# Performance work log

Measured on AMD Instinct MI355X. Metric: run time of the kernel, lower is better.

## Reference

```python
import jax, jax.numpy as jnp
import numpy as np
import math

BIG, SMALL, HEADS, FF_MULT = 4096, 256, 4, 2
HEAD_DIM = SMALL // HEADS
FF = SMALL * FF_MULT
EPS = 1.1920929e-07  # torch.nn.RMSNorm default eps=None -> finfo(float32).eps


def rmsnorm(x, g):
    var = jnp.mean(x * x, axis=-1, keepdims=True)
    return x * jax.lax.rsqrt(var + EPS) * g


def setup_inputs() -> dict:
    key = jax.random.key(0)
    ks = jax.random.split(key, 10)
    B, T = 4, 2048
    def lin(k, out_d, in_d):
        # torch nn.Linear default init: U(-1/sqrt(in), 1/sqrt(in)), weight shape (out, in)
        lim = 1.0 / math.sqrt(in_d)
        return jax.random.uniform(k, (out_d, in_d), jnp.float32, -lim, lim)
    return {
        "x": jax.random.normal(ks[0], (B, T, BIG), jnp.float32),
        "W_down": lin(ks[1], SMALL, BIG),
        "W_up": lin(ks[2], BIG, SMALL),
        "W_qkv": lin(ks[3], 3 * SMALL, SMALL),
        "W_o": lin(ks[4], SMALL, SMALL),
        "W_gate": lin(ks[5], FF, SMALL),
        "W_upff": lin(ks[6], FF, SMALL),
        "W_downff": lin(ks[7], SMALL, FF),
        "g1": jnp.ones((SMALL,), jnp.float32),
        "g2": jnp.ones((SMALL,), jnp.float32),
    }


def reference(x, W_down, W_up, W_qkv, W_o, W_gate, W_upff, W_downff, g1, g2):
    B, T, _ = x.shape
    h = x @ W_down.T                                     # (B,T,small)
    hn = rmsnorm(h, g1)
    qkv = (hn @ W_qkv.T).reshape(B, T, 3, HEADS, HEAD_DIM)
    qkv = jnp.transpose(qkv, (2, 0, 3, 1, 4))            # (3,B,H,T,hd)
    q, k, v = qkv[0], qkv[1], qkv[2]
    scores = jnp.einsum('bhqd,bhkd->bhqk', q, k) / math.sqrt(HEAD_DIM)
    causal = jnp.tril(jnp.ones((T, T), bool))
    scores = jnp.where(causal, scores, -jnp.inf)
    attn = jax.nn.softmax(scores, axis=-1)
    out = jnp.einsum('bhqk,bhkd->bhqd', attn, v)
    out = jnp.transpose(out, (0, 2, 1, 3)).reshape(B, T, SMALL)
    h = h + out @ W_o.T
    hn = rmsnorm(h, g2)
    ff = (jax.nn.silu(hn @ W_gate.T) * (hn @ W_upff.T)) @ W_downff.T
    h = h + ff
    return h @ W_up.T                                    # (B,T,big)
```

## Files before the change

### kernel.cpp

```cpp
#include <hip/hip_runtime.h>
#include <hip/hip_bf16.h>

typedef __bf16 bf16x8 __attribute__((ext_vector_type(8)));
typedef __bf16 bf16x4 __attribute__((ext_vector_type(4)));
typedef float f32x4 __attribute__((ext_vector_type(4)));

#define MFMA_BF16(a, b, c) __builtin_amdgcn_mfma_f32_16x16x32_bf16((a), (b), (c), 0, 0, 0)

__device__ __forceinline__ void g2lds16(void* lds, const void* g) {
  __builtin_amdgcn_global_load_lds(
      (const __attribute__((address_space(1))) void*)g,
      (__attribute__((address_space(3))) void*)lds, 16, 0, 0);
}

enum { EP_BF16 = 0, EP_F32 = 1, EP_ADD_F32 = 2, EP_ADD_BF16OUT = 3 };

template <int EPI, int MT, bool SPLITK = false>
__global__ __launch_bounds__(256, 2) void gemm_nt_kernel(
    const __bf16* __restrict__ A, const __bf16* __restrict__ B, const int K,
    __bf16* __restrict__ Co, float* __restrict__ Cf, const int ldc)
{
  __shared__ __align__(16) __bf16 As[2][MT * 32];
  __shared__ __align__(16) __bf16 Bs[2][128 * 32];
  const int tid = threadIdx.x;
  const int wv = tid >> 6, lane = tid & 63;
  const int r16 = lane & 15, g4 = lane >> 4;
  const int row0 = blockIdx.y * MT, col0 = blockIdx.x * 128;
  const int wr = (MT == 128) ? (wv >> 1) * 64 : 0;
  const int wc = (MT == 128) ? (wv & 1) * 64 : wv * 32;
  constexpr int NW = (MT == 128) ? 4 : 2;
  constexpr int NA = (MT == 128) ? 2 : 1;
  const int kz0 = SPLITK ? blockIdx.z * 1024 : 0;

  f32x4 acc[4][NW];
#pragma unroll
  for (int m = 0; m < 4; ++m)
#pragma unroll
    for (int n = 0; n < NW; ++n) acc[m][n] = f32x4{0.f, 0.f, 0.f, 0.f};

  auto stage = [&](int buf, int k0) {
#pragma unroll
    for (int rr = 0; rr < NA; ++rr) {
      const int u = rr * 256 + tid, row = u >> 2, cg = ((u & 3) ^ (row & 3)) * 8;
      g2lds16(&As[buf][u * 8], A + (size_t)(row0 + row) * K + k0 + cg);
    }
#pragma unroll
    for (int rr = 0; rr < 2; ++rr) {
      const int u = rr * 256 + tid, row = u >> 2, cg = ((u & 3) ^ (row & 3)) * 8;
      g2lds16(&Bs[buf][u * 8], B + (size_t)(col0 + row) * K + k0 + cg);
    }
  };

  const int nk = SPLITK ? 32 : (K >> 5);
  const int csw = (g4 ^ (r16 & 3)) * 8;
  int cur = 0;
  stage(0, kz0);
  __syncthreads();

  for (int t = 0; t < nk; ++t) {
    if (t + 1 < nk) stage(cur ^ 1, kz0 + (t + 1) * 32);
    bf16x8 af[4], bfr[NW];
#pragma unroll
    for (int m = 0; m < 4; ++m)
      af[m] = *(const bf16x8*)&As[cur][(wr + m * 16 + r16) * 32 + csw];
#pragma unroll
    for (int n = 0; n < NW; ++n)
      bfr[n] = *(const bf16x8*)&Bs[cur][(wc + n * 16 + r16) * 32 + csw];
#pragma unroll
    for (int m = 0; m < 4; ++m)
#pragma unroll
      for (int n = 0; n < NW; ++n)
        acc[m][n] = MFMA_BF16(af[m], bfr[n], acc[m][n]);
    __syncthreads();
    cur ^= 1;
  }

  const size_t zoff = SPLITK ? (size_t)blockIdx.z * 2097152 : 0;
#pragma unroll
  for (int m = 0; m < 4; ++m)
#pragma unroll
    for (int n = 0; n < NW; ++n)
#pragma unroll
      for (int r = 0; r < 4; ++r) {
        const int row = row0 + wr + m * 16 + g4 * 4 + r;
        const int col = col0 + wc + n * 16 + r16;
        const size_t idx = (size_t)row * ldc + col;
        const float v = acc[m][n][r];
        if constexpr (EPI == EP_BF16) Co[zoff + idx] = (__bf16)v;
        else if constexpr (EPI == EP_F32) __builtin_nontemporal_store(v, &Cf[idx]);
        else if constexpr (EPI == EP_ADD_F32) Cf[idx] += v;
        else Co[idx] = (__bf16)(Cf[idx] + v);
      }
}

__global__ __launch_bounds__(256, 2) void gemm_wo_kernel(
    const __bf16* __restrict__ opart, const float* __restrict__ lpart,
    const __bf16* __restrict__ B, float* __restrict__ Cf)
{
  __shared__ __align__(16) __bf16 As[2][64 * 32];
  __shared__ __align__(16) __bf16 Bs[2][128 * 32];
  const int tid = threadIdx.x;
  const int wv = tid >> 6, lane = tid & 63;
  const int r16 = lane & 15, g4 = lane >> 4;
  const int row0 = blockIdx.y * 64, col0 = blockIdx.x * 128;
  const int wc = wv * 32;

  f32x4 acc[4][2];
#pragma unroll
  for (int m = 0; m < 4; ++m)
#pragma unroll
    for (int n = 0; n < 2; ++n) acc[m][n] = f32x4{0.f, 0.f, 0.f, 0.f};

  const int arow = tid >> 2;
  const int R = row0 + arow;
  const int b = R >> 11, rr_ = R & 2047;
  const int qb = rr_ >> 6, rloc = rr_ & 63;
  const int cgrp = ((tid & 3) ^ (arow & 3)) * 8;

  auto stageA = [&](int buf, int t) {
    const int hh = t >> 1;
    const int dbase = (t & 1) * 32 + cgrp;
    const size_t pb = ((size_t)((b * 4 + hh) * 32 + qb)) * 2;
    const bf16x8 o0 = *(const bf16x8*)(opart + pb * 4096 + rloc * 64 + dbase);
    const bf16x8 o1 = *(const bf16x8*)(opart + (pb + 1) * 4096 + rloc * 64 + dbase);
    const float inv = 1.f / (lpart[pb * 64 + rloc] + lpart[(pb + 1) * 64 + rloc]);
    bf16x8 w;
#pragma unroll
    for (int j = 0; j < 8; ++j) w[j] = (__bf16)(((float)o0[j] + (float)o1[j]) * inv);
    *(bf16x8*)&As[buf][tid * 8] = w;
  };
  auto stageB = [&](int buf, int k0) {
#pragma unroll
    for (int rr = 0; rr < 2; ++rr) {
      const int u = rr * 256 + tid, row = u >> 2, cg = ((u & 3) ^ (row & 3)) * 8;
      g2lds16(&Bs[buf][u * 8], B + (size_t)(col0 + row) * 256 + k0 + cg);
    }
  };

  const int csw = (g4 ^ (r16 & 3)) * 8;
  int cur = 0;
  stageA(0, 0);
  stageB(0, 0);
  __syncthreads();

  for (int t = 0; t < 8; ++t) {
    if (t + 1 < 8) { stageA(cur ^ 1, t + 1); stageB(cur ^ 1, (t + 1) * 32); }
    bf16x8 af[4], bfr[2];
#pragma unroll
    for (int m = 0; m < 4; ++m)
      af[m] = *(const bf16x8*)&As[cur][(m * 16 + r16) * 32 + csw];
#pragma unroll
    for (int n = 0; n < 2; ++n)
      bfr[n] = *(const bf16x8*)&Bs[cur][(wc + n * 16 + r16) * 32 + csw];
#pragma unroll
    for (int m = 0; m < 4; ++m)
#pragma unroll
      for (int n = 0; n < 2; ++n)
        acc[m][n] = MFMA_BF16(af[m], bfr[n], acc[m][n]);
    __syncthreads();
    cur ^= 1;
  }

#pragma unroll
  for (int m = 0; m < 4; ++m)
#pragma unroll
    for (int n = 0; n < 2; ++n)
#pragma unroll
      for (int r = 0; r < 4; ++r) {
        const int row = row0 + m * 16 + g4 * 4 + r;
        const int col = col0 + wc + n * 16 + r16;
        Cf[(size_t)row * 256 + col] += acc[m][n][r];
      }
}

__global__ void cvt_x_kernel(const float* __restrict__ src, __bf16* __restrict__ dst)
{
  const int stride = gridDim.x * 256;
  for (size_t i = (size_t)blockIdx.x * 256 + threadIdx.x; i < 8388608; i += stride) {
    const f32x4 v = *(const f32x4*)(src + i * 4);
    bf16x4 o;
#pragma unroll
    for (int j = 0; j < 4; ++j) o[j] = (__bf16)v[j];
    *(bf16x4*)(dst + i * 4) = o;
  }
}

__global__ void rmsnorm_reduce_kernel(const __bf16* __restrict__ part, const float* __restrict__ g,
                                      float* __restrict__ h, __bf16* __restrict__ out)
{
  const int wv = threadIdx.x >> 6, lane = threadIdx.x & 63;
  const size_t row = (size_t)blockIdx.x * 4 + wv;
  const size_t i = row * 256 + lane * 4;
  f32x4 v = {0.f, 0.f, 0.f, 0.f};
#pragma unroll
  for (int z = 0; z < 4; ++z) {
    const bf16x4 p = *(const bf16x4*)(part + (size_t)z * 2097152 + i);
#pragma unroll
    for (int j = 0; j < 4; ++j) v[j] += (float)p[j];
  }
  *(f32x4*)(h + i) = v;
  float s = v[0] * v[0] + v[1] * v[1] + v[2] * v[2] + v[3] * v[3];
#pragma unroll
  for (int off = 1; off < 64; off <<= 1) s += __shfl_xor(s, off);
  const float scale = rsqrtf(s * (1.f / 256.f) + 1.1920929e-07f);
  const f32x4 gv = *(const f32x4*)(g + lane * 4);
  bf16x4 o;
#pragma unroll
  for (int j = 0; j < 4; ++j) o[j] = (__bf16)(v[j] * scale * gv[j]);
  *(bf16x4*)(out + i) = o;
}

__global__ void rmsnorm_kernel(const float* __restrict__ h, const float* __restrict__ g,
                               __bf16* __restrict__ out)
{
  const int wv = threadIdx.x >> 6, lane = threadIdx.x & 63;
  const size_t row = (size_t)blockIdx.x * 4 + wv;
  const f32x4 v = *(const f32x4*)(h + row * 256 + lane * 4);
  float s = v[0] * v[0] + v[1] * v[1] + v[2] * v[2] + v[3] * v[3];
#pragma unroll
  for (int off = 1; off < 64; off <<= 1) s += __shfl_xor(s, off);
  const float scale = rsqrtf(s * (1.f / 256.f) + 1.1920929e-07f);
  const f32x4 gv = *(const f32x4*)(g + lane * 4);
  bf16x4 o;
#pragma unroll
  for (int j = 0; j < 4; ++j) o[j] = (__bf16)(v[j] * scale * gv[j]);
  *(bf16x4*)(out + row * 256 + lane * 4) = o;
}

struct CvtPack { const float* s[7]; __bf16* d[7]; int n[7]; };
__global__ void cvt_all_kernel(CvtPack p)
{
  int i = (blockIdx.x * 256 + threadIdx.x) * 4;
#pragma unroll
  for (int k = 0; k < 7; ++k) {
    if (i < p.n[k]) {
      const f32x4 v = *(const f32x4*)(p.s[k] + i);
      bf16x4 o;
#pragma unroll
      for (int j = 0; j < 4; ++j) o[j] = (__bf16)v[j];
      *(bf16x4*)(p.d[k] + i) = o;
      return;
    }
    i -= p.n[k];
  }
}

__global__ void silumul_kernel(const __bf16* __restrict__ gu, __bf16* __restrict__ out)
{
  const int gid = blockIdx.x * 256 + threadIdx.x;
  const int row = gid >> 6, k = (gid & 63) * 8;
  const bf16x8 gv = *(const bf16x8*)(gu + (size_t)row * 1024 + k);
  const bf16x8 uv = *(const bf16x8*)(gu + (size_t)row * 1024 + 512 + k);
  bf16x8 ov;
#pragma unroll
  for (int j = 0; j < 8; ++j) {
    const float x = (float)gv[j];
    ov[j] = (__bf16)((x / (1.f + __expf(-x))) * (float)uv[j]);
  }
  *(bf16x8*)(out + (size_t)row * 512 + k) = ov;
}

__global__ __launch_bounds__(256, 4) void attn_kernel(
    const __bf16* __restrict__ qkv, __bf16* __restrict__ opart, float* __restrict__ lpart)
{
  const int bh = blockIdx.x;
  const int by = blockIdx.y;
  const int qb = (by < 16) ? (31 - by) : (by - 16);
  const int z = blockIdx.z;
  const int b = bh >> 2, hh = bh & 3;
  const int tid = threadIdx.x, wv = tid >> 6, lane = tid & 63;
  const int r16 = lane & 15, g4 = lane >> 4;
  const __bf16* base = qkv + (size_t)b * 2048 * 768;
  const int q0 = qb * 64;

  __shared__ __align__(16) __bf16 Ks[2][64 * 64];
  __shared__ __align__(16) __bf16 Vt[64 * 72];
  __shared__ __align__(16) __bf16 Ps[4][16 * 72];

  bf16x8 qf[2];
  {
    const __bf16* qrow = base + (size_t)(q0 + wv * 16 + r16) * 768 + hh * 64;
    qf[0] = *(const bf16x8*)(qrow + g4 * 8);
    qf[1] = *(const bf16x8*)(qrow + 32 + g4 * 8);
  }

  f32x4 oacc[4];
#pragma unroll
  for (int t = 0; t < 4; ++t) oacc[t] = f32x4{0.f, 0.f, 0.f, 0.f};
  float lsum[4] = {0.f, 0.f, 0.f, 0.f};

  auto stageK = [&](int buf, int kv0) {
#pragma unroll
    for (int rr = 0; rr < 2; ++rr) {
      const int u = rr * 256 + tid;
      const int kv = u >> 3, c = u & 7;
      g2lds16(&Ks[buf][u * 8],
              base + (size_t)(kv0 + kv) * 768 + 256 + hh * 64 + ((c ^ (kv & 7)) * 8));
    }
  };
  const int vrow = tid >> 2, vdg = (tid & 3) * 16;
  const int va_ = vrow >> 3, vb_ = vrow & 7;

  bf16x8 v0r, v1r;
  auto loadV = [&](int kv0) {
    const __bf16* vsrc = base + (size_t)(kv0 + vrow) * 768 + 512 + hh * 64 + vdg;
    v0r = *(const bf16x8*)vsrc;
    v1r = *(const bf16x8*)(vsrc + 8);
  };
  auto writeVt = [&]() {
#pragma unroll
    for (int i = 0; i < 8; ++i) {
      int d = vdg + i;
      Vt[d * 72 + ((va_ ^ (d >> 3)) << 3) + vb_] = v0r[i];
      d = vdg + 8 + i;
      Vt[d * 72 + ((va_ ^ (d >> 3)) << 3) + vb_] = v1r[i];
    }
  };

  int c = z, cur = 0;
  const bool any = (c <= qb);
  if (any) { stageK(0, c * 64); loadV(c * 64); }
  __syncthreads();
  if (any) writeVt();
  __syncthreads();

  while (c <= qb) {
    const int nxt = c + 2;
    if (nxt <= qb) { stageK(cur ^ 1, nxt * 64); loadV(nxt * 64); }

    f32x4 sacc[4];
#pragma unroll
    for (int t = 0; t < 4; ++t) sacc[t] = f32x4{0.f, 0.f, 0.f, 0.f};
#pragma unroll
    for (int t = 0; t < 4; ++t)
#pragma unroll
      for (int kk = 0; kk < 2; ++kk) {
        const bf16x8 kf = *(const bf16x8*)
            &Ks[cur][(t * 16 + r16) * 64 + (((kk * 4 + g4) ^ (r16 & 7)) * 8)];
        sacc[t] = MFMA_BF16(qf[kk], kf, sacc[t]);
      }

    const bool diag = (c == qb);
#pragma unroll
    for (int t = 0; t < 4; ++t)
#pragma unroll
      for (int r = 0; r < 4; ++r) {
        float p = __expf(sacc[t][r] * 0.125f);
        if (diag && (t * 16 + r16 > wv * 16 + g4 * 4 + r)) p = 0.f;
        lsum[r] += p;
        Ps[wv][(g4 * 4 + r) * 72 + t * 16 + r16] = (__bf16)p;
      }
    bf16x8 pa[2];
    pa[0] = *(const bf16x8*)&Ps[wv][r16 * 72 + g4 * 8];
    pa[1] = *(const bf16x8*)&Ps[wv][r16 * 72 + 32 + g4 * 8];

#pragma unroll
    for (int t2 = 0; t2 < 4; ++t2)
#pragma unroll
      for (int kk = 0; kk < 2; ++kk) {
        const int d = t2 * 16 + r16;
        const bf16x8 vf = *(const bf16x8*)
            &Vt[d * 72 + (((kk * 4 + g4) ^ (d >> 3)) * 8)];
        oacc[t2] = MFMA_BF16(pa[kk], vf, oacc[t2]);
      }

    __syncthreads();
    if (nxt <= qb) writeVt();
    __syncthreads();
    c = nxt;
    cur ^= 1;
  }

#pragma unroll
  for (int r = 0; r < 4; ++r) {
    lsum[r] += __shfl_xor(lsum[r], 1);
    lsum[r] += __shfl_xor(lsum[r], 2);
    lsum[r] += __shfl_xor(lsum[r], 4);
    lsum[r] += __shfl_xor(lsum[r], 8);
  }
  const size_t pb = (size_t)(bh * 32 + qb) * 2 + z;
  __bf16* op = opart + pb * 4096;
#pragma unroll
  for (int t2 = 0; t2 < 4; ++t2)
#pragma unroll
    for (int r = 0; r < 4; ++r)
      op[(wv * 16 + g4 * 4 + r) * 64 + t2 * 16 + r16] = (__bf16)oacc[t2][r];
  if (r16 == 0) {
    float* lp = lpart + pb * 64;
#pragma unroll
    for (int r = 0; r < 4; ++r) lp[wv * 16 + g4 * 4 + r] = lsum[r];
  }
}

extern "C" void kernel_launch(void* const* d_in, const int* in_sizes, int n_in,
                              void* d_out, int out_size, void* d_ws, size_t ws_size,
                              hipStream_t stream) {
  (void)in_sizes; (void)n_in; (void)out_size; (void)ws_size;
  const float* x     = (const float*)d_in[0];
  const float* Wdown = (const float*)d_in[1];
  const float* Wup   = (const float*)d_in[2];
  const float* Wqkv  = (const float*)d_in[3];
  const float* Wo    = (const float*)d_in[4];
  const float* Wgate = (const float*)d_in[5];
  const float* Wupff = (const float*)d_in[6];
  const float* Wdff  = (const float*)d_in[7];
  const float* g1    = (const float*)d_in[8];
  const float* g2    = (const float*)d_in[9];
  float* out = (float*)d_out;

  const size_t MB = 1 << 20;
  char* ws = (char*)d_ws;
  float*  h  = (float*)ws;
  __bf16* hn = (__bf16*)(ws + 8 * MB);
  __bf16* hb = (__bf16*)(ws + 12 * MB);
  __bf16* wb_down = (__bf16*)(ws + 16 * MB);
  __bf16* wb_up   = (__bf16*)(ws + 18 * MB);
  __bf16* wb_qkv  = (__bf16*)(ws + 20 * MB);
  __bf16* wb_o    = (__bf16*)(ws + 20 * MB + 384 * 1024);
  __bf16* wb_gate = (__bf16*)(ws + 20 * MB + 512 * 1024);
  __bf16* wb_upff = (__bf16*)(ws + 20 * MB + 768 * 1024);
  __bf16* wb_dff  = (__bf16*)(ws + 21 * MB);

  char* ob = (char*)d_out;
  __bf16* xb    = (__bf16*)(ob);
  __bf16* hpart = (__bf16*)(ob + 64 * MB);
  __bf16* qkv   = (__bf16*)(ob);
  __bf16* gu    = (__bf16*)(ob + 12 * MB);
  __bf16* ffmid = (__bf16*)(ob + 28 * MB);
  __bf16* opart = (__bf16*)(ob + 36 * MB);
  float* lpart  = (float*)(ob + 53 * MB);

  CvtPack cp;
  cp.s[0] = Wdown; cp.d[0] = wb_down; cp.n[0] = 1048576;
  cp.s[1] = Wup;   cp.d[1] = wb_up;   cp.n[1] = 1048576;
  cp.s[2] = Wqkv;  cp.d[2] = wb_qkv;  cp.n[2] = 196608;
  cp.s[3] = Wo;    cp.d[3] = wb_o;    cp.n[3] = 65536;
  cp.s[4] = Wgate; cp.d[4] = wb_gate; cp.n[4] = 131072;
  cp.s[5] = Wupff; cp.d[5] = wb_upff; cp.n[5] = 131072;
  cp.s[6] = Wdff;  cp.d[6] = wb_dff;  cp.n[6] = 131072;
  cvt_all_kernel<<<2688, 256, 0, stream>>>(cp);

  cvt_x_kernel<<<2048, 256, 0, stream>>>(x, xb);
  gemm_nt_kernel<EP_BF16, 128, true><<<dim3(2, 64, 4), 256, 0, stream>>>(
      xb, wb_down, 4096, hpart, nullptr, 256);
  rmsnorm_reduce_kernel<<<2048, 256, 0, stream>>>(hpart, g1, h, hn);

  gemm_nt_kernel<EP_BF16, 64><<<dim3(6, 128), 256, 0, stream>>>(
      hn, wb_qkv, 256, qkv, nullptr, 768);
  attn_kernel<<<dim3(16, 32, 2), 256, 0, stream>>>(qkv, opart, lpart);
  gemm_wo_kernel<<<dim3(2, 128), 256, 0, stream>>>(opart, lpart, wb_o, h);
  rmsnorm_kernel<<<2048, 256, 0, stream>>>(h, g2, hn);
  gemm_nt_kernel<EP_BF16, 64><<<dim3(8, 128), 256, 0, stream>>>(
      hn, wb_gate, 256, gu, nullptr, 1024);
  silumul_kernel<<<2048, 256, 0, stream>>>(gu, ffmid);
  gemm_nt_kernel<EP_ADD_BF16OUT, 64><<<dim3(2, 128), 256, 0, stream>>>(
      ffmid, wb_dff, 512, hb, h, 256);
  gemm_nt_kernel<EP_F32, 128><<<dim3(32, 64), 256, 0, stream>>>(
      hb, wb_up, 256, nullptr, out, 4096);
}
```

Before: 204.2 us.

## Fuse SiLU-mul into dual gate/up GEMM and merge x conversion into weight cvt

Adds a GEMM kernel that computes the gate and up projections together and applies SiLU-multiply in the epilogue, removing the intermediate gu buffer and the separate silumul kernel. The fp32-to-bf16 conversion of x is folded into the packed weight conversion launch. The Wo and down-ff GEMMs use 32-row tiles for more blocks, and gemm_nt raises its occupancy hint to 4. The trade-off is more register and LDS pressure in the fused kernel, and half-idle threads when staging A for the 32-row tiles.

```diff
diff --git a/kernel.cpp b/kernel.cpp
--- a/kernel.cpp
+++ b/kernel.cpp
@@ -16,7 +16,7 @@
 enum { EP_BF16 = 0, EP_F32 = 1, EP_ADD_F32 = 2, EP_ADD_BF16OUT = 3 };
 
 template <int EPI, int MT, bool SPLITK = false>
-__global__ __launch_bounds__(256, 2) void gemm_nt_kernel(
+__global__ __launch_bounds__(256, 4) void gemm_nt_kernel(
     const __bf16* __restrict__ A, const __bf16* __restrict__ B, const int K,
     __bf16* __restrict__ Co, float* __restrict__ Cf, const int ldc)
 {
@@ -29,20 +29,27 @@
   const int wr = (MT == 128) ? (wv >> 1) * 64 : 0;
   const int wc = (MT == 128) ? (wv & 1) * 64 : wv * 32;
   constexpr int NW = (MT == 128) ? 4 : 2;
-  constexpr int NA = (MT == 128) ? 2 : 1;
+  constexpr int MFR = (MT >= 64) ? 4 : 2;
   const int kz0 = SPLITK ? blockIdx.z * 1024 : 0;
 
-  f32x4 acc[4][NW];
-#pragma unroll
-  for (int m = 0; m < 4; ++m)
+  f32x4 acc[MFR][NW];
+#pragma unroll
+  for (int m = 0; m < MFR; ++m)
 #pragma unroll
     for (int n = 0; n < NW; ++n) acc[m][n] = f32x4{0.f, 0.f, 0.f, 0.f};
 
   auto stage = [&](int buf, int k0) {
-#pragma unroll
-    for (int rr = 0; rr < NA; ++rr) {
-      const int u = rr * 256 + tid, row = u >> 2, cg = ((u & 3) ^ (row & 3)) * 8;
-      g2lds16(&As[buf][u * 8], A + (size_t)(row0 + row) * K + k0 + cg);
+    if constexpr (MT == 32) {
+      if (tid < 128) {
+        const int u = tid, row = u >> 2, cg = ((u & 3) ^ (row & 3)) * 8;
+        g2lds16(&As[buf][u * 8], A + (size_t)(row0 + row) * K + k0 + cg);
+      }
+    } else {
+#pragma unroll
+      for (int rr = 0; rr < MT / 64; ++rr) {
+        const int u = rr * 256 + tid, row = u >> 2, cg = ((u & 3) ^ (row & 3)) * 8;
+        g2lds16(&As[buf][u * 8], A + (size_t)(row0 + row) * K + k0 + cg);
+      }
     }
 #pragma unroll
     for (int rr = 0; rr < 2; ++rr) {
@@ -59,15 +66,15 @@
 
   for (int t = 0; t < nk; ++t) {
     if (t + 1 < nk) stage(cur ^ 1, kz0 + (t + 1) * 32);
-    bf16x8 af[4], bfr[NW];
-#pragma unroll
-    for (int m = 0; m < 4; ++m)
+    bf16x8 af[MFR], bfr[NW];
+#pragma unroll
+    for (int m = 0; m < MFR; ++m)
       af[m] = *(const bf16x8*)&As[cur][(wr + m * 16 + r16) * 32 + csw];
 #pragma unroll
     for (int n = 0; n < NW; ++n)
       bfr[n] = *(const bf16x8*)&Bs[cur][(wc + n * 16 + r16) * 32 + csw];
 #pragma unroll
-    for (int m = 0; m < 4; ++m)
+    for (int m = 0; m < MFR; ++m)
 #pragma unroll
       for (int n = 0; n < NW; ++n)
         acc[m][n] = MFMA_BF16(af[m], bfr[n], acc[m][n]);
@@ -77,7 +84,7 @@
 
   const size_t zoff = SPLITK ? (size_t)blockIdx.z * 2097152 : 0;
 #pragma unroll
-  for (int m = 0; m < 4; ++m)
+  for (int m = 0; m < MFR; ++m)
 #pragma unroll
     for (int n = 0; n < NW; ++n)
 #pragma unroll
@@ -93,41 +100,119 @@
       }
 }
 
-__global__ __launch_bounds__(256, 2) void gemm_wo_kernel(
-    const __bf16* __restrict__ opart, const float* __restrict__ lpart,
-    const __bf16* __restrict__ B, float* __restrict__ Cf)
+__global__ __launch_bounds__(256, 2) void gemm_gu_kernel(
+    const __bf16* __restrict__ A, const __bf16* __restrict__ Bg,
+    const __bf16* __restrict__ Bu, __bf16* __restrict__ ffmid)
 {
   __shared__ __align__(16) __bf16 As[2][64 * 32];
-  __shared__ __align__(16) __bf16 Bs[2][128 * 32];
+  __shared__ __align__(16) __bf16 Bgs[2][128 * 32];
+  __shared__ __align__(16) __bf16 Bus[2][128 * 32];
   const int tid = threadIdx.x;
   const int wv = tid >> 6, lane = tid & 63;
   const int r16 = lane & 15, g4 = lane >> 4;
   const int row0 = blockIdx.y * 64, col0 = blockIdx.x * 128;
   const int wc = wv * 32;
 
-  f32x4 acc[4][2];
+  f32x4 accG[4][2], accU[4][2];
 #pragma unroll
   for (int m = 0; m < 4; ++m)
 #pragma unroll
+    for (int n = 0; n < 2; ++n) {
+      accG[m][n] = f32x4{0.f, 0.f, 0.f, 0.f};
+      accU[m][n] = f32x4{0.f, 0.f, 0.f, 0.f};
+    }
+
+  auto stage = [&](int buf, int k0) {
+    {
+      const int u = tid, row = u >> 2, cg = ((u & 3) ^ (row & 3)) * 8;
+      g2lds16(&As[buf][u * 8], A + (size_t)(row0 + row) * 256 + k0 + cg);
+    }
+#pragma unroll
+    for (int rr = 0; rr < 2; ++rr) {
+      const int u = rr * 256 + tid, row = u >> 2, cg = ((u & 3) ^ (row & 3)) * 8;
+      g2lds16(&Bgs[buf][u * 8], Bg + (size_t)(col0 + row) * 256 + k0 + cg);
+      g2lds16(&Bus[buf][u * 8], Bu + (size_t)(col0 + row) * 256 + k0 + cg);
+    }
+  };
+
+  const int csw = (g4 ^ (r16 & 3)) * 8;
+  int cur = 0;
+  stage(0, 0);
+  __syncthreads();
+
+  for (int t = 0; t < 8; ++t) {
+    if (t + 1 < 8) stage(cur ^ 1, (t + 1) * 32);
+    bf16x8 af[4], bg[2], bu[2];
+#pragma unroll
+    for (int m = 0; m < 4; ++m)
+      af[m] = *(const bf16x8*)&As[cur][(m * 16 + r16) * 32 + csw];
+#pragma unroll
+    for (int n = 0; n < 2; ++n) {
+      bg[n] = *(const bf16x8*)&Bgs[cur][(wc + n * 16 + r16) * 32 + csw];
+      bu[n] = *(const bf16x8*)&Bus[cur][(wc + n * 16 + r16) * 32 + csw];
+    }
+#pragma unroll
+    for (int m = 0; m < 4; ++m)
+#pragma unroll
+      for (int n = 0; n < 2; ++n) {
+        accG[m][n] = MFMA_BF16(af[m], bg[n], accG[m][n]);
+        accU[m][n] = MFMA_BF16(af[m], bu[n], accU[m][n]);
+      }
+    __syncthreads();
+    cur ^= 1;
+  }
+
+#pragma unroll
+  for (int m = 0; m < 4; ++m)
+#pragma unroll
+    for (int n = 0; n < 2; ++n)
+#pragma unroll
+      for (int r = 0; r < 4; ++r) {
+        const int row = row0 + m * 16 + g4 * 4 + r;
+        const int col = col0 + wc + n * 16 + r16;
+        const float g = accG[m][n][r];
+        const float u = accU[m][n][r];
+        ffmid[(size_t)row * 512 + col] = (__bf16)((g / (1.f + __expf(-g))) * u);
+      }
+}
+
+__global__ __launch_bounds__(256, 2) void gemm_wo_kernel(
+    const __bf16* __restrict__ opart, const float* __restrict__ lpart,
+    const __bf16* __restrict__ B, float* __restrict__ Cf)
+{
+  __shared__ __align__(16) __bf16 As[2][32 * 32];
+  __shared__ __align__(16) __bf16 Bs[2][128 * 32];
+  const int tid = threadIdx.x;
+  const int wv = tid >> 6, lane = tid & 63;
+  const int r16 = lane & 15, g4 = lane >> 4;
+  const int row0 = blockIdx.y * 32, col0 = blockIdx.x * 128;
+  const int wc = wv * 32;
+
+  f32x4 acc[2][2];
+#pragma unroll
+  for (int m = 0; m < 2; ++m)
+#pragma unroll
     for (int n = 0; n < 2; ++n) acc[m][n] = f32x4{0.f, 0.f, 0.f, 0.f};
 
   const int arow = tid >> 2;
-  const int R = row0 + arow;
+  const int R = row0 + (arow & 31);
   const int b = R >> 11, rr_ = R & 2047;
   const int qb = rr_ >> 6, rloc = rr_ & 63;
   const int cgrp = ((tid & 3) ^ (arow & 3)) * 8;
 
   auto stageA = [&](int buf, int t) {
-    const int hh = t >> 1;
-    const int dbase = (t & 1) * 32 + cgrp;
-    const size_t pb = ((size_t)((b * 4 + hh) * 32 + qb)) * 2;
-    const bf16x8 o0 = *(const bf16x8*)(opart + pb * 4096 + rloc * 64 + dbase);
-    const bf16x8 o1 = *(const bf16x8*)(opart + (pb + 1) * 4096 + rloc * 64 + dbase);
-    const float inv = 1.f / (lpart[pb * 64 + rloc] + lpart[(pb + 1) * 64 + rloc]);
-    bf16x8 w;
-#pragma unroll
-    for (int j = 0; j < 8; ++j) w[j] = (__bf16)(((float)o0[j] + (float)o1[j]) * inv);
-    *(bf16x8*)&As[buf][tid * 8] = w;
+    if (tid < 128) {
+      const int hh = t >> 1;
+      const int dbase = (t & 1) * 32 + cgrp;
+      const size_t pb = ((size_t)((b * 4 + hh) * 32 + qb)) * 2;
+      const bf16x8 o0 = *(const bf16x8*)(opart + pb * 4096 + rloc * 64 + dbase);
+      const bf16x8 o1 = *(const bf16x8*)(opart + (pb + 1) * 4096 + rloc * 64 + dbase);
+      const float inv = 1.f / (lpart[pb * 64 + rloc] + lpart[(pb + 1) * 64 + rloc]);
+      bf16x8 w;
+#pragma unroll
+      for (int j = 0; j < 8; ++j) w[j] = (__bf16)(((float)o0[j] + (float)o1[j]) * inv);
+      *(bf16x8*)&As[buf][tid * 8] = w;
+    }
   };
   auto stageB = [&](int buf, int k0) {
 #pragma unroll
@@ -145,15 +230,15 @@
 
   for (int t = 0; t < 8; ++t) {
     if (t + 1 < 8) { stageA(cur ^ 1, t + 1); stageB(cur ^ 1, (t + 1) * 32); }
-    bf16x8 af[4], bfr[2];
-#pragma unroll
-    for (int m = 0; m < 4; ++m)
+    bf16x8 af[2], bfr[2];
+#pragma unroll
+    for (int m = 0; m < 2; ++m)
       af[m] = *(const bf16x8*)&As[cur][(m * 16 + r16) * 32 + csw];
 #pragma unroll
     for (int n = 0; n < 2; ++n)
       bfr[n] = *(const bf16x8*)&Bs[cur][(wc + n * 16 + r16) * 32 + csw];
 #pragma unroll
-    for (int m = 0; m < 4; ++m)
+    for (int m = 0; m < 2; ++m)
 #pragma unroll
       for (int n = 0; n < 2; ++n)
         acc[m][n] = MFMA_BF16(af[m], bfr[n], acc[m][n]);
@@ -162,7 +247,7 @@
   }
 
 #pragma unroll
-  for (int m = 0; m < 4; ++m)
+  for (int m = 0; m < 2; ++m)
 #pragma unroll
     for (int n = 0; n < 2; ++n)
 #pragma unroll
@@ -173,18 +258,6 @@
       }
 }
 
-__global__ void cvt_x_kernel(const float* __restrict__ src, __bf16* __restrict__ dst)
-{
-  const int stride = gridDim.x * 256;
-  for (size_t i = (size_t)blockIdx.x * 256 + threadIdx.x; i < 8388608; i += stride) {
-    const f32x4 v = *(const f32x4*)(src + i * 4);
-    bf16x4 o;
-#pragma unroll
-    for (int j = 0; j < 4; ++j) o[j] = (__bf16)v[j];
-    *(bf16x4*)(dst + i * 4) = o;
-  }
-}
-
 __global__ void rmsnorm_reduce_kernel(const __bf16* __restrict__ part, const float* __restrict__ g,
                                       float* __restrict__ h, __bf16* __restrict__ out)
 {
@@ -227,12 +300,12 @@
   *(bf16x4*)(out + row * 256 + lane * 4) = o;
 }
 
-struct CvtPack { const float* s[7]; __bf16* d[7]; int n[7]; };
+struct CvtPack { const float* s[8]; __bf16* d[8]; int n[8]; };
 __global__ void cvt_all_kernel(CvtPack p)
 {
   int i = (blockIdx.x * 256 + threadIdx.x) * 4;
 #pragma unroll
-  for (int k = 0; k < 7; ++k) {
+  for (int k = 0; k < 8; ++k) {
     if (i < p.n[k]) {
       const f32x4 v = *(const f32x4*)(p.s[k] + i);
       bf16x4 o;
@@ -243,21 +316,6 @@
     }
     i -= p.n[k];
   }
-}
-
-__global__ void silumul_kernel(const __bf16* __restrict__ gu, __bf16* __restrict__ out)
-{
-  const int gid = blockIdx.x * 256 + threadIdx.x;
-  const int row = gid >> 6, k = (gid & 63) * 8;
-  const bf16x8 gv = *(const bf16x8*)(gu + (size_t)row * 1024 + k);
-  const bf16x8 uv = *(const bf16x8*)(gu + (size_t)row * 1024 + 512 + k);
-  bf16x8 ov;
-#pragma unroll
-  for (int j = 0; j < 8; ++j) {
-    const float x = (float)gv[j];
-    ov[j] = (__bf16)((x / (1.f + __expf(-x))) * (float)uv[j]);
-  }
-  *(bf16x8*)(out + (size_t)row * 512 + k) = ov;
 }
 
 __global__ __launch_bounds__(256, 4) void attn_kernel(
@@ -425,8 +483,7 @@
   __bf16* xb    = (__bf16*)(ob);
   __bf16* hpart = (__bf16*)(ob + 64 * MB);
   __bf16* qkv   = (__bf16*)(ob);
-  __bf16* gu    = (__bf16*)(ob + 12 * MB);
-  __bf16* ffmid = (__bf16*)(ob + 28 * MB);
+  __bf16* ffmid = (__bf16*)(ob + 12 * MB);
   __bf16* opart = (__bf16*)(ob + 36 * MB);
   float* lpart  = (float*)(ob + 53 * MB);
 
@@ -438,9 +495,9 @@
   cp.s[4] = Wgate; cp.d[4] = wb_gate; cp.n[4] = 131072;
   cp.s[5] = Wupff; cp.d[5] = wb_upff; cp.n[5] = 131072;
   cp.s[6] = Wdff;  cp.d[6] = wb_dff;  cp.n[6] = 131072;
-  cvt_all_kernel<<<2688, 256, 0, stream>>>(cp);
-
-  cvt_x_kernel<<<2048, 256, 0, stream>>>(x, xb);
+  cp.s[7] = x;     cp.d[7] = xb;      cp.n[7] = 33554432;
+  cvt_all_kernel<<<35456, 256, 0, stream>>>(cp);
+
   gemm_nt_kernel<EP_BF16, 128, true><<<dim3(2, 64, 4), 256, 0, stream>>>(
       xb, wb_down, 4096, hpart, nullptr, 256);
   rmsnorm_reduce_kernel<<<2048, 256, 0, stream>>>(hpart, g1, h, hn);
@@ -448,12 +505,10 @@
   gemm_nt_kernel<EP_BF16, 64><<<dim3(6, 128), 256, 0, stream>>>(
       hn, wb_qkv, 256, qkv, nullptr, 768);
   attn_kernel<<<dim3(16, 32, 2), 256, 0, stream>>>(qkv, opart, lpart);
-  gemm_wo_kernel<<<dim3(2, 128), 256, 0, stream>>>(opart, lpart, wb_o, h);
+  gemm_wo_kernel<<<dim3(2, 256), 256, 0, stream>>>(opart, lpart, wb_o, h);
   rmsnorm_kernel<<<2048, 256, 0, stream>>>(h, g2, hn);
-  gemm_nt_kernel<EP_BF16, 64><<<dim3(8, 128), 256, 0, stream>>>(
-      hn, wb_gate, 256, gu, nullptr, 1024);
-  silumul_kernel<<<2048, 256, 0, stream>>>(gu, ffmid);
-  gemm_nt_kernel<EP_ADD_BF16OUT, 64><<<dim3(2, 128), 256, 0, stream>>>(
+  gemm_gu_kernel<<<dim3(4, 128), 256, 0, stream>>>(hn, wb_gate, wb_upff, ffmid);
+  gemm_nt_kernel<EP_ADD_BF16OUT, 32><<<dim3(2, 256), 256, 0, stream>>>(
       ffmid, wb_dff, 512, hb, h, 256);
   gemm_nt_kernel<EP_F32, 128><<<dim3(32, 64), 256, 0, stream>>>(
       hb, wb_up, 256, nullptr, out, 4096);
```

Result: faster. 195.8 us (-4.1%).
